# Kernel tuning notes

Hardware: AMD Instinct MI355X
Metric: run time of the kernel (lower is better)

The kernel has to match this reference:

```python
import jax, jax.numpy as jnp
import numpy as np


def setup_inputs() -> dict:
    key = jax.random.key(0)
    k1, k2 = jax.random.split(key)
    D = 32            # num_detectors
    IN_S = 64         # input_size per detector
    OUT_S = 64        # output_size per detector
    B = 8192          # batch
    x = jax.random.normal(k1, (B, IN_S * D), dtype=jnp.float32)
    # nn.Linear weight: [out_features, in_features] = [OUT_S*D, IN_S*D]
    W = jax.random.normal(k2, (OUT_S * D, IN_S * D), dtype=jnp.float32) * (1.0 / np.sqrt(IN_S * D))
    return {"x": x, "W": W, "num_detectors": D}


def reference(x, W, num_detectors):
    # Original: y = ((W * block_diag_mask) @ x.T).T
    # The mask zeroes everything except num_detectors diagonal (out_s, in_s)
    # blocks, so this is exactly num_detectors independent linears. We compute
    # only the diagonal blocks (same math; off-diagonal weights contribute 0).
    D = num_detectors
    total_out, total_in = W.shape
    out_s = total_out // D
    in_s = total_in // D
    # extract diagonal blocks -> [D, out_s, in_s]
    Wb = W.reshape(D, out_s, D, in_s)
    d = jnp.arange(D)
    blocks = Wb[d, :, d, :]                      # [D, out_s, in_s]
    xb = x.reshape(x.shape[0], D, in_s)          # [B, D, in_s]
    y = jnp.einsum('bdi,doi->bdo', xb, blocks)   # [B, D, out_s]
    return y.reshape(x.shape[0], D * out_s)
```

## Files before the change

kernel.cpp:

```cpp
#include <hip/hip_runtime.h>

#define NDET    32
#define SEG     64
#define ROWLEN  2048
#define DGRP    4
#define XCOLS   (DGRP * SEG)
#define TILE_R  64
#define THREADS 256
#define XLSTR   264
#define WLSTR   72

typedef __bf16 bf16x8 __attribute__((ext_vector_type(8)));
typedef __bf16 bf16x4 __attribute__((ext_vector_type(4)));
typedef float  f32x4  __attribute__((ext_vector_type(4)));

__device__ __forceinline__ bf16x4 cvt4(f32x4 a) {
  bf16x4 r;
  r[0] = (__bf16)a[0]; r[1] = (__bf16)a[1]; r[2] = (__bf16)a[2]; r[3] = (__bf16)a[3];
  return r;
}

__global__ __launch_bounds__(THREADS) void ensemble_linear_v8(
    const float* __restrict__ x, const float* __restrict__ W,
    float* __restrict__ y) {
  const int dg     = blockIdx.y;
  const int dbase0 = dg * XCOLS;
  const int r0     = blockIdx.x * TILE_R;
  const int t      = threadIdx.x;
  const int lane   = t & 63;
  const int wid    = t >> 6;
  const int rq  = lane >> 4;
  const int c4  = lane & 15;
  const int m16 = lane & 15;
  const int kg  = lane >> 4;

  __shared__ __bf16 xls[TILE_R * XLSTR];
  __shared__ __bf16 wls[DGRP * SEG * WLSTR];

  f32x4 xv[16];
#pragma unroll
  for (int p = 0; p < 16; ++p) {
    const int row = p * 4 + wid;
    xv[p] = *(const f32x4*)(x + (size_t)(r0 + row) * ROWLEN + dbase0 + lane * 4);
  }

  f32x4 wv[16];
#pragma unroll
  for (int p = 0; p < 16; ++p) {
    const int o = p * 4 + rq;
    wv[p] = *(const f32x4*)(W + (size_t)(dbase0 + wid * SEG + o) * ROWLEN
                              + dbase0 + wid * SEG + c4 * 4);
  }

#pragma unroll
  for (int p = 0; p < 16; ++p) {
    const int row = p * 4 + wid;
    *(bf16x4*)(&xls[row * XLSTR + lane * 4]) = cvt4(xv[p]);
  }
#pragma unroll
  for (int p = 0; p < 16; ++p) {
    const int o = p * 4 + rq;
    *(bf16x4*)(&wls[(wid * SEG + o) * WLSTR + c4 * 4]) = cvt4(wv[p]);
  }

  __syncthreads();

  const int rbase = wid * 16;
#pragma unroll
  for (int q = 0; q < DGRP; ++q) {
    bf16x8 a0 = *(const bf16x8*)(&xls[(rbase + m16) * XLSTR + q * SEG + kg * 8]);
    bf16x8 a1 = *(const bf16x8*)(&xls[(rbase + m16) * XLSTR + q * SEG + 32 + kg * 8]);

    float* yp = y + (size_t)(r0 + rbase + m16) * ROWLEN + dbase0 + q * SEG + kg * 4;
#pragma unroll
    for (int g = 0; g < 4; ++g) {
      bf16x8 w0 = *(const bf16x8*)(&wls[(q * SEG + g * 16 + m16) * WLSTR + kg * 8]);
      bf16x8 w1 = *(const bf16x8*)(&wls[(q * SEG + g * 16 + m16) * WLSTR + 32 + kg * 8]);
      f32x4 acc = (f32x4){0.f, 0.f, 0.f, 0.f};
      acc = __builtin_amdgcn_mfma_f32_16x16x32_bf16(w0, a0, acc, 0, 0, 0);
      acc = __builtin_amdgcn_mfma_f32_16x16x32_bf16(w1, a1, acc, 0, 0, 0);
      *(f32x4*)(yp + g * 16) = acc;
    }
  }
}

extern "C" void kernel_launch(void* const* d_in, const int* in_sizes, int n_in,
                              void* d_out, int out_size, void* d_ws, size_t ws_size,
                              hipStream_t stream) {
  const float* x = (const float*)d_in[0];
  const float* W = (const float*)d_in[1];
  float* y = (float*)d_out;
  const int B = in_sizes[0] / ROWLEN;
  dim3 grid(B / TILE_R, NDET / DGRP);
  ensemble_linear_v8<<<grid, dim3(THREADS), 0, stream>>>(x, W, y);
}
```

Measured before the change: 29.56 us.

## Stage output through LDS for coalesced row stores and reassign waves per detector

After: 27.22 us. -7.9%, faster.

```diff
diff --git a/kernel.cpp b/kernel.cpp
--- a/kernel.cpp
+++ b/kernel.cpp
@@ -9,6 +9,7 @@
 #define THREADS 256
 #define XLSTR   264
 #define WLSTR   72
+#define YLSTR   260
 
 typedef __bf16 bf16x8 __attribute__((ext_vector_type(8)));
 typedef __bf16 bf16x4 __attribute__((ext_vector_type(4)));
@@ -20,7 +21,7 @@
   return r;
 }
 
-__global__ __launch_bounds__(THREADS) void ensemble_linear_v8(
+__global__ __launch_bounds__(THREADS) void ensemble_linear_v10(
     const float* __restrict__ x, const float* __restrict__ W,
     float* __restrict__ y) {
   const int dg     = blockIdx.y;
@@ -34,8 +35,10 @@
   const int m16 = lane & 15;
   const int kg  = lane >> 4;
 
-  __shared__ __bf16 xls[TILE_R * XLSTR];
-  __shared__ __bf16 wls[DGRP * SEG * WLSTR];
+  __shared__ __align__(16) unsigned char smem[TILE_R * XLSTR * 2 + DGRP * SEG * WLSTR * 2];
+  __bf16* xls = (__bf16*)smem;
+  __bf16* wls = (__bf16*)(smem + TILE_R * XLSTR * 2);
+  float*  yls = (float*)smem;
 
   f32x4 xv[16];
 #pragma unroll
@@ -65,22 +68,43 @@
 
   __syncthreads();
 
-  const int rbase = wid * 16;
+  bf16x8 wfrag[4][2];
 #pragma unroll
-  for (int q = 0; q < DGRP; ++q) {
-    bf16x8 a0 = *(const bf16x8*)(&xls[(rbase + m16) * XLSTR + q * SEG + kg * 8]);
-    bf16x8 a1 = *(const bf16x8*)(&xls[(rbase + m16) * XLSTR + q * SEG + 32 + kg * 8]);
+  for (int g = 0; g < 4; ++g)
+#pragma unroll
+    for (int kh = 0; kh < 2; ++kh)
+      wfrag[g][kh] = *(const bf16x8*)(
+          &wls[(wid * SEG + g * 16 + m16) * WLSTR + kh * 32 + kg * 8]);
 
-    float* yp = y + (size_t)(r0 + rbase + m16) * ROWLEN + dbase0 + q * SEG + kg * 4;
+  bf16x8 afrag[4][2];
+#pragma unroll
+  for (int s = 0; s < 4; ++s) {
+#pragma unroll
+    for (int kh = 0; kh < 2; ++kh)
+      afrag[s][kh] = *(const bf16x8*)(
+          &xls[(s * 16 + m16) * XLSTR + wid * SEG + kh * 32 + kg * 8]);
+  }
+
+  __syncthreads();
+
+#pragma unroll
+  for (int s = 0; s < 4; ++s) {
 #pragma unroll
     for (int g = 0; g < 4; ++g) {
-      bf16x8 w0 = *(const bf16x8*)(&wls[(q * SEG + g * 16 + m16) * WLSTR + kg * 8]);
-      bf16x8 w1 = *(const bf16x8*)(&wls[(q * SEG + g * 16 + m16) * WLSTR + 32 + kg * 8]);
       f32x4 acc = (f32x4){0.f, 0.f, 0.f, 0.f};
-      acc = __builtin_amdgcn_mfma_f32_16x16x32_bf16(w0, a0, acc, 0, 0, 0);
-      acc = __builtin_amdgcn_mfma_f32_16x16x32_bf16(w1, a1, acc, 0, 0, 0);
-      *(f32x4*)(yp + g * 16) = acc;
+      acc = __builtin_amdgcn_mfma_f32_16x16x32_bf16(wfrag[g][0], afrag[s][0], acc, 0, 0, 0);
+      acc = __builtin_amdgcn_mfma_f32_16x16x32_bf16(wfrag[g][1], afrag[s][1], acc, 0, 0, 0);
+      *(f32x4*)(&yls[(s * 16 + m16) * YLSTR + wid * SEG + g * 16 + kg * 4]) = acc;
     }
+  }
+
+  __syncthreads();
+
+#pragma unroll
+  for (int p = 0; p < 16; ++p) {
+    const int row = p * 4 + wid;
+    f32x4 v = *(const f32x4*)(&yls[row * YLSTR + lane * 4]);
+    *(f32x4*)(y + (size_t)(r0 + row) * ROWLEN + dbase0 + lane * 4) = v;
   }
 }
 
@@ -92,5 +116,5 @@
   float* y = (float*)d_out;
   const int B = in_sizes[0] / ROWLEN;
   dim3 grid(B / TILE_R, NDET / DGRP);
-  ensemble_linear_v8<<<grid, dim3(THREADS), 0, stream>>>(x, W, y);
+  ensemble_linear_v10<<<grid, dim3(THREADS), 0, stream>>>(x, W, y);
 }
```
